# Kernel tuning notes

Hardware: AMD Instinct MI355X
Metric: run time of the kernel (lower is better)

## Reference

```python
import jax, jax.numpy as jnp
import numpy as np

B, N, E = 2, 16000, 160000
NDIMS, NMEAS, NMODES = 2, 1, 128
IN_DIM, OUT_DIM, FC_DIM = 3, 1, 128
LAYERS = [64, 64, 64, 64]
INV_MIN, INV_MAX = 0.5, 2.0


def setup_inputs() -> dict:
    key = jax.random.key(0)
    ks = jax.random.split(key, 16)
    L = len(LAYERS) - 1
    C = LAYERS[0]
    scale = 1.0 / (C * C)
    u = lambda k, sh, s: jax.random.uniform(k, sh, jnp.float32, -s, s)
    inp = {}
    inp["x"] = jax.random.normal(ks[0], (B, N, IN_DIM), jnp.float32)
    inp["node_mask"] = jnp.ones((B, N, 1), jnp.int32)
    inp["nodes"] = jax.random.uniform(ks[1], (B, N, NDIMS), jnp.float32)
    inp["node_weights"] = jax.random.uniform(ks[2], (B, N, NMEAS), jnp.float32) / N
    inp["directed_edges"] = jax.random.randint(ks[3], (B, E, 2), 0, N, jnp.int32)
    inp["edge_gradient_weights"] = jax.random.normal(ks[4], (B, E, NDIMS), jnp.float32)
    inp["modes"] = jax.random.normal(ks[5], (NMODES, NDIMS, NMEAS), jnp.float32)
    # scaled_logit(1.0, 0.5, 2.0) = log(0.5/1.0)
    inp["inv_L_scale_latent"] = jnp.full((NDIMS, NMEAS), np.log((1.0 - INV_MIN) / (INV_MAX - 1.0)), jnp.float32)
    inp["fc0_W"] = u(ks[6], (C, IN_DIM), 1.0 / np.sqrt(IN_DIM))
    inp["fc0_b"] = jnp.zeros((C,), jnp.float32)
    inp["weights_c"] = u(ks[7], (L, C, C, NMODES, NMEAS), scale)
    inp["weights_s"] = u(ks[8], (L, C, C, NMODES, NMEAS), scale)
    inp["weights_0"] = u(ks[9], (L, C, C, 1, NMEAS), scale)
    inp["ws_W"] = u(ks[10], (L, C, C), 1.0 / np.sqrt(C))
    inp["ws_b"] = jnp.zeros((L, C), jnp.float32)
    inp["gws_W"] = u(ks[11], (L, C, C * NDIMS), 1.0 / np.sqrt(C * NDIMS))
    inp["gws_b"] = jnp.zeros((L, C), jnp.float32)
    inp["fc1_W"] = u(ks[12], (FC_DIM, C), 1.0 / np.sqrt(C))
    inp["fc1_b"] = jnp.zeros((FC_DIM,), jnp.float32)
    inp["fc2_W"] = u(ks[13], (OUT_DIM, FC_DIM), 1.0 / np.sqrt(FC_DIM))
    inp["fc2_b"] = jnp.zeros((OUT_DIM,), jnp.float32)
    return inp


def _forward(x, nodes, node_weights, edge_gradient_weights, modes, inv_L_scale_latent,
             fc0_W, fc0_b, weights_c, weights_s, weights_0, ws_W, ws_b, gws_W, gws_b,
             fc1_W, fc1_b, fc2_W, fc2_b, directed_edges):
    L = weights_c.shape[0]
    n = x.shape[1]
    # scaled sigmoid of latent inverse length scale
    inv_L = INV_MIN + (INV_MAX - INV_MIN) * jax.nn.sigmoid(inv_L_scale_latent)
    smodes = modes * inv_L  # [K, D, W]
    # Fourier bases over all nodes
    temp = jnp.einsum('bxd,kdw->bxkw', nodes, smodes)  # [B, N, K, W]
    bases_c, bases_s = jnp.cos(temp), jnp.sin(temp)
    bases_0 = jnp.ones(temp.shape[:2] + (1, temp.shape[-1]), temp.dtype)
    wnw = node_weights[:, :, None, :]  # [B, N, 1, W]
    wbases_c, wbases_s, wbases_0 = bases_c * wnw, bases_s * wnw, bases_0 * wnw

    tgt = directed_edges[..., 0]  # [B, E]
    src = directed_edges[..., 1]

    def grad_field(f):  # f: [B, C, N] -> [B, C*D, N]
        ft = jnp.transpose(f, (0, 2, 1))  # [B, N, C]
        f_src = jnp.take_along_axis(ft, src[..., None], axis=1)  # [B, E, C]
        f_tgt = jnp.take_along_axis(ft, tgt[..., None], axis=1)
        diff = f_src - f_tgt
        msg = jnp.einsum('bed,bec->becd', edge_gradient_weights, diff)  # [B, E, C, D]
        msg = msg.reshape(msg.shape[0], msg.shape[1], -1)  # [B, E, C*D]
        seg = jax.vmap(lambda m, t: jax.ops.segment_sum(m, t, num_segments=n))(msg, tgt)
        return jnp.transpose(seg, (0, 2, 1))  # [B, C*D, N]

    # lift: fc0 acts on channel dim
    h = jnp.einsum('oi,bni->bon', fc0_W, x) + fc0_b[None, :, None]  # [B, C, N]

    for i in range(L):
        # spectral conv with explicit bases
        x_c = jnp.einsum('bix,bxkw->bikw', h, wbases_c)
        x_s = -jnp.einsum('bix,bxkw->bikw', h, wbases_s)
        x_0 = jnp.einsum('bix,bxkw->bikw', h, wbases_0)
        f_c = jnp.einsum('bikw,iokw->bokw', x_c, weights_c[i]) - jnp.einsum('bikw,iokw->bokw', x_s, weights_s[i])
        f_s = jnp.einsum('bikw,iokw->bokw', x_s, weights_c[i]) + jnp.einsum('bikw,iokw->bokw', x_c, weights_s[i])
        f_0 = jnp.einsum('bikw,iokw->bokw', x_0, weights_0[i])
        x1 = (jnp.einsum('bokw,bxkw->box', f_0, bases_0)
              + 2 * jnp.einsum('bokw,bxkw->box', f_c, bases_c)
              - 2 * jnp.einsum('bokw,bxkw->box', f_s, bases_s))
        # pointwise linear W
        x2 = jnp.einsum('oi,bin->bon', ws_W[i], h) + ws_b[i][None, :, None]
        # differential operator D: gradient then linear
        x3 = jnp.einsum('oi,bin->bon', gws_W[i], grad_field(h)) + gws_b[i][None, :, None]
        h = x1 + x2 + x3
        if i < L - 1:
            h = jax.nn.gelu(h)

    out = jnp.transpose(h, (0, 2, 1))  # [B, N, C]
    out = jax.nn.gelu(jnp.einsum('oc,bnc->bno', fc1_W, out) + fc1_b)
    out = jnp.einsum('oc,bnc->bno', fc2_W, out) + fc2_b
    return out  # [B, N, out_dim]


def reference(x, node_mask, nodes, node_weights, directed_edges, edge_gradient_weights,
              modes, inv_L_scale_latent, fc0_W, fc0_b, weights_c, weights_s, weights_0,
              ws_W, ws_b, gws_W, gws_b, fc1_W, fc1_b, fc2_W, fc2_b):
    del node_mask  # padding mask; all-ones here, not used in the core math
    return _forward(x, nodes, node_weights, edge_gradient_weights, modes, inv_L_scale_latent,
                    fc0_W, fc0_b, weights_c, weights_s, weights_0, ws_W, ws_b, gws_W, gws_b,
                    fc1_W, fc1_b, fc2_W, fc2_b, directed_edges)
```

## Files before the change

### kernel.cpp

```cpp
#include <hip/hip_runtime.h>
#include <math.h>

#define BB 2
#define NN 16000
#define EE 160000
#define KK 128
#define CC 64
#define LL 3

typedef __attribute__((ext_vector_type(8))) short bf16x8;
typedef __attribute__((ext_vector_type(4))) float f32x4;

__device__ __forceinline__ float gelu_f(float x){
    float x3 = x * x * x;
    return 0.5f * x * (1.f + tanhf(0.7978845608028654f * (x + 0.044715f * x3)));
}
__device__ __forceinline__ ushort f2bf(float f){
    uint u = __float_as_uint(f);
    u += 0x7fff + ((u >> 16) & 1);
    return (ushort)(u >> 16);
}
__device__ __forceinline__ float bf2f(ushort h){ return __uint_as_float(((uint)h) << 16); }
__device__ __forceinline__ void fsplit(float v, ushort &hi, ushort &lo){
    hi = f2bf(v);
    lo = f2bf(v - bf2f(hi));
}
__device__ __forceinline__ uint pk2(ushort a, ushort b){ return (uint)a | ((uint)b << 16); }

__global__ __launch_bounds__(256) void k_bases(
    const float* __restrict__ nodes, const float* __restrict__ modes,
    const float* __restrict__ latent, const float* __restrict__ nw,
    ushort* __restrict__ cbh, ushort* __restrict__ cbl,
    ushort* __restrict__ sbh, ushort* __restrict__ sbl,
    ushort* __restrict__ wTh, ushort* __restrict__ wTl){
    int bid = blockIdx.x;
    int b = bid / 250, x0 = (bid % 250) * 64;
    int t = threadIdx.x;
    __shared__ float sm0[128], sm1[128], nwv[64];
    __shared__ uint tc[64][65], ts[64][65];
    if (t < 128){
        float i0 = 0.5f + 1.5f / (1.f + expf(-latent[0]));
        float i1 = 0.5f + 1.5f / (1.f + expf(-latent[1]));
        sm0[t] = modes[t*2+0] * i0;
        sm1[t] = modes[t*2+1] * i1;
    }
    if (t < 64) nwv[t] = nw[b*NN + x0 + t];
    __syncthreads();
    int xloc = t & 63;
    float n0 = nodes[((size_t)b*NN + x0 + xloc)*2 + 0];
    float n1 = nodes[((size_t)b*NN + x0 + xloc)*2 + 1];
    for (int kh = 0; kh < 2; kh++){
        int kq = t >> 6;
        #pragma unroll
        for (int j = 0; j < 16; j++){
            int kl = kq*16 + j;
            int k = kh*64 + kl;
            float tmp = n0*sm0[k] + n1*sm1[k];
            float sv, cv; sincosf(tmp, &sv, &cv);
            ushort h_, l_;
            fsplit(cv, h_, l_); tc[xloc][kl] = pk2(h_, l_);
            fsplit(sv, h_, l_); ts[xloc][kl] = pk2(h_, l_);
        }
        __syncthreads();
        {
            int q = t >> 6;
            size_t base = ((size_t)b*NN + x0 + xloc)*128 + kh*64 + q*16;
            #pragma unroll
            for (int g2 = 0; g2 < 2; g2++){
                uint u0 = tc[xloc][q*16 + g2*8 + 0], u1 = tc[xloc][q*16 + g2*8 + 1];
                uint u2 = tc[xloc][q*16 + g2*8 + 2], u3 = tc[xloc][q*16 + g2*8 + 3];
                uint u4 = tc[xloc][q*16 + g2*8 + 4], u5 = tc[xloc][q*16 + g2*8 + 5];
                uint u6 = tc[xloc][q*16 + g2*8 + 6], u7 = tc[xloc][q*16 + g2*8 + 7];
                uint4 vh, vl;
                vh.x = pk2((ushort)u0,(ushort)u1); vh.y = pk2((ushort)u2,(ushort)u3);
                vh.z = pk2((ushort)u4,(ushort)u5); vh.w = pk2((ushort)u6,(ushort)u7);
                vl.x = pk2((ushort)(u0>>16),(ushort)(u1>>16)); vl.y = pk2((ushort)(u2>>16),(ushort)(u3>>16));
                vl.z = pk2((ushort)(u4>>16),(ushort)(u5>>16)); vl.w = pk2((ushort)(u6>>16),(ushort)(u7>>16));
                *(uint4*)&cbh[base + g2*8] = vh;
                *(uint4*)&cbl[base + g2*8] = vl;
                u0 = ts[xloc][q*16 + g2*8 + 0]; u1 = ts[xloc][q*16 + g2*8 + 1];
                u2 = ts[xloc][q*16 + g2*8 + 2]; u3 = ts[xloc][q*16 + g2*8 + 3];
                u4 = ts[xloc][q*16 + g2*8 + 4]; u5 = ts[xloc][q*16 + g2*8 + 5];
                u6 = ts[xloc][q*16 + g2*8 + 6]; u7 = ts[xloc][q*16 + g2*8 + 7];
                vh.x = pk2((ushort)u0,(ushort)u1); vh.y = pk2((ushort)u2,(ushort)u3);
                vh.z = pk2((ushort)u4,(ushort)u5); vh.w = pk2((ushort)u6,(ushort)u7);
                vl.x = pk2((ushort)(u0>>16),(ushort)(u1>>16)); vl.y = pk2((ushort)(u2>>16),(ushort)(u3>>16));
                vl.z = pk2((ushort)(u4>>16),(ushort)(u5>>16)); vl.w = pk2((ushort)(u6>>16),(ushort)(u7>>16));
                *(uint4*)&sbh[base + g2*8] = vh;
                *(uint4*)&sbl[base + g2*8] = vl;
            }
        }
        {
            int k = t & 63, g = t >> 6;
            int kgc = kh*64 + k;
            int kgs = 128 + kh*64 + k;
            ushort hc[16], lc[16], hs[16], ls[16];
            #pragma unroll
            for (int j = 0; j < 16; j++){
                int xx = g*16 + j;
                float wgt = nwv[xx];
                uint uc = tc[xx][k], us = ts[xx][k];
                float vc = (bf2f((ushort)uc) + bf2f((ushort)(uc>>16))) * wgt;
                float vs = (bf2f((ushort)us) + bf2f((ushort)(us>>16))) * wgt;
                fsplit(vc, hc[j], lc[j]);
                fsplit(vs, hs[j], ls[j]);
            }
            size_t wbc = ((size_t)b*256 + kgc)*16000 + x0 + g*16;
            size_t wbs = ((size_t)b*256 + kgs)*16000 + x0 + g*16;
            uint4 v;
            v.x = pk2(hc[0],hc[1]); v.y = pk2(hc[2],hc[3]); v.z = pk2(hc[4],hc[5]); v.w = pk2(hc[6],hc[7]);
            *(uint4*)&wTh[wbc] = v;
            v.x = pk2(hc[8],hc[9]); v.y = pk2(hc[10],hc[11]); v.z = pk2(hc[12],hc[13]); v.w = pk2(hc[14],hc[15]);
            *(uint4*)&wTh[wbc + 8] = v;
            v.x = pk2(lc[0],lc[1]); v.y = pk2(lc[2],lc[3]); v.z = pk2(lc[4],lc[5]); v.w = pk2(lc[6],lc[7]);
            *(uint4*)&wTl[wbc] = v;
            v.x = pk2(lc[8],lc[9]); v.y = pk2(lc[10],lc[11]); v.z = pk2(lc[12],lc[13]); v.w = pk2(lc[14],lc[15]);
            *(uint4*)&wTl[wbc + 8] = v;
            v.x = pk2(hs[0],hs[1]); v.y = pk2(hs[2],hs[3]); v.z = pk2(hs[4],hs[5]); v.w = pk2(hs[6],hs[7]);
            *(uint4*)&wTh[wbs] = v;
            v.x = pk2(hs[8],hs[9]); v.y = pk2(hs[10],hs[11]); v.z = pk2(hs[12],hs[13]); v.w = pk2(hs[14],hs[15]);
            *(uint4*)&wTh[wbs + 8] = v;
            v.x = pk2(ls[0],ls[1]); v.y = pk2(ls[2],ls[3]); v.z = pk2(ls[4],ls[5]); v.w = pk2(ls[6],ls[7]);
            *(uint4*)&wTl[wbs] = v;
            v.x = pk2(ls[8],ls[9]); v.y = pk2(ls[10],ls[11]); v.z = pk2(ls[12],ls[13]); v.w = pk2(ls[14],ls[15]);
            *(uint4*)&wTl[wbs + 8] = v;
        }
        __syncthreads();
    }
}

__device__ __forceinline__ void write_h_outputs(
    const float* ot, const float* nws, int b, int s, int x0, int t, int doAux,
    float* __restrict__ hx, ushort* __restrict__ hxh, ushort* __restrict__ hxl,
    ushort* __restrict__ hwh, ushort* __restrict__ hwl, float* __restrict__ part0){
    {
        int xl = t >> 1, half = t & 1;
        size_t gb = ((size_t)b*NN + x0 + xl)*64 + half*32;
        const float* row = &ot[xl*68 + half*32];
        #pragma unroll
        for (int j = 0; j < 8; j++){
            float4 v; v.x = row[j*4]; v.y = row[j*4+1]; v.z = row[j*4+2]; v.w = row[j*4+3];
            *(float4*)&hx[gb + j*4] = v;
        }
        if (doAux){
            #pragma unroll
            for (int q = 0; q < 4; q++){
                ushort h_[8], l_[8];
                #pragma unroll
                for (int j = 0; j < 8; j++) fsplit(row[q*8 + j], h_[j], l_[j]);
                uint4 vh, vl;
                vh.x = pk2(h_[0],h_[1]); vh.y = pk2(h_[2],h_[3]); vh.z = pk2(h_[4],h_[5]); vh.w = pk2(h_[6],h_[7]);
                vl.x = pk2(l_[0],l_[1]); vl.y = pk2(l_[2],l_[3]); vl.z = pk2(l_[4],l_[5]); vl.w = pk2(l_[6],l_[7]);
                *(uint4*)&hxh[gb + q*8] = vh;
                *(uint4*)&hxl[gb + q*8] = vl;
            }
        }
    }
    if (doAux){
        int i = t & 63, g = t >> 6;
        float a = 0.f;
        #pragma unroll
        for (int rep = 0; rep < 4; rep++){
            int xs = g*32 + rep*8;
            ushort h_[8], l_[8];
            #pragma unroll
            for (int j = 0; j < 8; j++){
                float v = ot[(xs + j)*68 + i] * nws[xs + j];
                a += v;
                fsplit(v, h_[j], l_[j]);
            }
            uint4 vh, vl;
            vh.x = pk2(h_[0],h_[1]); vh.y = pk2(h_[2],h_[3]); vh.z = pk2(h_[4],h_[5]); vh.w = pk2(h_[6],h_[7]);
            vl.x = pk2(l_[0],l_[1]); vl.y = pk2(l_[2],l_[3]); vl.z = pk2(l_[4],l_[5]); vl.w = pk2(l_[6],l_[7]);
            size_t wb = (size_t)(b*64 + i)*16000 + x0 + xs;
            *(uint4*)&hwh[wb] = vh;
            *(uint4*)&hwl[wb] = vl;
        }
        part0[((size_t)(b*125 + s)*4 + g)*64 + i] = a;
    }
}

__global__ __launch_bounds__(256) void k_fc0(
    const float* __restrict__ x, const float* __restrict__ W,
    const float* __restrict__ bb, const float* __restrict__ nw,
    float* __restrict__ hx, ushort* __restrict__ hxh, ushort* __restrict__ hxl,
    ushort* __restrict__ hwh, ushort* __restrict__ hwl, float* __restrict__ part0){
    int bid = blockIdx.x;
    int b = bid / 125, s = bid % 125;
    int x0 = s * 128;
    int t = threadIdx.x;
    __shared__ float ot[128*68];
    __shared__ float nws[128];
    __shared__ float Wf[192], bf_[64];
    if (t < 192) Wf[t] = W[t];
    if (t < 64) bf_[t] = bb[t];
    if (t < 128) nws[t] = nw[b*NN + x0 + t];
    __syncthreads();
    {
        int xl = t >> 1, half = t & 1;
        float v0 = x[((size_t)b*NN + x0 + xl)*3 + 0];
        float v1 = x[((size_t)b*NN + x0 + xl)*3 + 1];
        float v2 = x[((size_t)b*NN + x0 + xl)*3 + 2];
        #pragma unroll
        for (int j = 0; j < 32; j++){
            int o = half*32 + j;
            ot[xl*68 + o] = Wf[o*3]*v0 + Wf[o*3+1]*v1 + Wf[o*3+2]*v2 + bf_[o];
        }
    }
    __syncthreads();
    write_h_outputs(ot, nws, b, s, x0, t, 1, hx, hxh, hxl, hwh, hwl, part0);
}

__global__ __launch_bounds__(256) void csr_hist(
    const int* __restrict__ edges, int* __restrict__ cnt){
    int idx = blockIdx.x * 256 + threadIdx.x;
    if (idx >= BB*EE) return;
    int b = idx / EE;
    int tgt = edges[(size_t)idx*2];
    atomicAdd(&cnt[b*NN + tgt], 1);
}

__global__ __launch_bounds__(1024) void csr_scan(
    const int* __restrict__ cnt, int* __restrict__ rowptr, int* __restrict__ cursor){
    int b = blockIdx.x;
    int t = threadIdx.x;
    __shared__ int lds[1024];
    int base = t * 16;
    int v[16];
    int run = 0;
    #pragma unroll
    for (int j = 0; j < 16; j++){
        int n = base + j;
        int c = (n < NN) ? cnt[b*NN + n] : 0;
        v[j] = run;
        run += c;
    }
    lds[t] = run;
    __syncthreads();
    for (int off = 1; off < 1024; off <<= 1){
        int xv = (t >= off) ? lds[t-off] : 0;
        __syncthreads();
        lds[t] += xv;
        __syncthreads();
    }
    int toff = lds[t] - run;
    #pragma unroll
    for (int j = 0; j < 16; j++){
        int n = base + j;
        if (n < NN){
            int p = toff + v[j];
            rowptr[b*(NN+1) + n] = p;
            cursor[b*NN + n] = p;
        }
    }
    if (t == 1023) rowptr[b*(NN+1) + NN] = lds[1023];
}

__global__ __launch_bounds__(256) void csr_fill(
    const int* __restrict__ edges, const float* __restrict__ egw,
    int* __restrict__ cursor, int* __restrict__ insrc, float2* __restrict__ inw){
    int idx = blockIdx.x * 256 + threadIdx.x;
    if (idx >= BB*EE) return;
    int b = idx / EE;
    int tgt = edges[(size_t)idx*2];
    int src = edges[(size_t)idx*2 + 1];
    int pos = atomicAdd(&cursor[b*NN + tgt], 1);
    insrc[(size_t)b*EE + pos] = src;
    const float2 wv = *(const float2*)&egw[(size_t)idx*2];
    inw[(size_t)b*EE + pos] = wv;
}

__global__ __launch_bounds__(256) void k1_fwd(
    const ushort* __restrict__ hwH, const ushort* __restrict__ hwL,
    const ushort* __restrict__ wTH, const ushort* __restrict__ wTL,
    float* __restrict__ part){
    int bid = blockIdx.x;
    int b = bid / 250, s = bid % 250;
    int x0 = s * 64;
    int t = threadIdx.x, l = t & 63, w = t >> 6;
    __shared__ __align__(16) ushort Bh[128*64], Bl[128*64];
    f32x4 acc[16] = {};
    bf16x8 Ah[2], Al[2];
    int i = w*16 + (l & 15);
    #pragma unroll
    for (int ks = 0; ks < 2; ks++){
        size_t ab = (size_t)(b*64 + i)*16000 + x0 + ks*32 + ((l >> 4) * 8);
        Ah[ks] = *reinterpret_cast<const bf16x8*>(&hwH[ab]);
        Al[ks] = *reinterpret_cast<const bf16x8*>(&hwL[ab]);
    }
    for (int p = 0; p < 2; p++){
        #pragma unroll
        for (int it = 0; it < 4; it++){
            int u = it*256 + t;
            int kloc = u >> 3, q = u & 7;
            size_t g = ((size_t)(b*256 + p*128 + kloc))*16000 + x0 + q*8;
            uint4 vh = *(const uint4*)&wTH[g];
            uint4 vl = *(const uint4*)&wTL[g];
            int ldsb = kloc*128 + ((q*16) ^ ((kloc & 7) << 4));
            *(uint4*)&Bh[ldsb >> 1] = vh;
            *(uint4*)&Bl[ldsb >> 1] = vl;
        }
        __syncthreads();
        #pragma unroll
        for (int kt = 0; kt < 8; kt++){
            int kcol = kt*16 + (l & 15);
            int ai = p*8 + kt;
            #pragma unroll
            for (int ks = 0; ks < 2; ks++){
                int boff = kcol*128 + (((ks*64) + ((l >> 4) * 16)) ^ ((kcol & 7) << 4));
                bf16x8 bh = *reinterpret_cast<const bf16x8*>(&Bh[boff >> 1]);
                bf16x8 bl = *reinterpret_cast<const bf16x8*>(&Bl[boff >> 1]);
                acc[ai] = __builtin_amdgcn_mfma_f32_16x16x32_bf16(Ah[ks], bh, acc[ai], 0, 0, 0);
                acc[ai] = __builtin_amdgcn_mfma_f32_16x16x32_bf16(Ah[ks], bl, acc[ai], 0, 0, 0);
                acc[ai] = __builtin_amdgcn_mfma_f32_16x16x32_bf16(Al[ks], bh, acc[ai], 0, 0, 0);
            }
        }
        __syncthreads();
    }
    size_t pb = (size_t)(b*250 + s) * 64 * 256;
    #pragma unroll
    for (int nt = 0; nt < 16; nt++){
        #pragma unroll
        for (int r = 0; r < 4; r++){
            int irow = w*16 + (l >> 4)*4 + r;
            part[pb + (size_t)irow*256 + nt*16 + (l & 15)] = acc[nt][r];
        }
    }
}

__global__ __launch_bounds__(512) void k1_reduce(
    const float* __restrict__ part, float* __restrict__ Sc, float* __restrict__ Ss){
    int b = blockIdx.x >> 6, i = blockIdx.x & 63;
    int t = threadIdx.x;
    int c = t & 255, sh = t >> 8;
    float a0=0,a1=0,a2=0,a3=0;
    int j = sh;
    for (; j + 6 < 250; j += 8){
        a0 += part[((size_t)(b*250 + j    )*64 + i)*256 + c];
        a1 += part[((size_t)(b*250 + j + 2)*64 + i)*256 + c];
        a2 += part[((size_t)(b*250 + j + 4)*64 + i)*256 + c];
        a3 += part[((size_t)(b*250 + j + 6)*64 + i)*256 + c];
    }
    for (; j < 250; j += 2)
        a0 += part[((size_t)(b*250 + j)*64 + i)*256 + c];
    float sum = (a0+a1)+(a2+a3);
    __shared__ float r2[256];
    if (sh) r2[c] = sum;
    __syncthreads();
    if (!sh){
        sum += r2[c];
        if (c < 128) Sc[(size_t)(b*64 + i)*128 + c] = sum;
        else         Ss[(size_t)(b*64 + i)*128 + (c - 128)] = sum;
    }
}

__global__ __launch_bounds__(256) void k2_mix(
    const float* __restrict__ Sc, const float* __restrict__ Ss,
    const float* __restrict__ part0,
    const float* __restrict__ wc, const float* __restrict__ wsp,
    const float* __restrict__ w0,
    const float* __restrict__ wsb, const float* __restrict__ gwsb,
    const float* __restrict__ wsW, const float* __restrict__ gwsW,
    ushort* __restrict__ WbH, ushort* __restrict__ WbL,
    float* __restrict__ bias, int l){
    int b = blockIdx.x >> 6, o = blockIdx.x & 63;
    int t = threadIdx.x;
    __shared__ float fc2s[2][128], fs2s[2][128];
    __shared__ float red[64];
    if (t < 64){
        float x0 = 0.f;
        for (int s2 = 0; s2 < 500; s2++) x0 += part0[(size_t)(b*500 + s2)*64 + t];
        red[t] = x0 * w0[((size_t)l*CC + t)*CC + o];
    }
    int k = t & 127, hf = t >> 7;
    float fc = 0.f, fs = 0.f;
    for (int i = hf*32; i < hf*32 + 32; i++){
        float sc = Sc[(size_t)(b*CC + i)*KK + k];
        float ss = Ss[(size_t)(b*CC + i)*KK + k];
        size_t wi = (((size_t)l*CC + i)*CC + o)*KK + k;
        float a = wc[wi], bb2 = wsp[wi];
        fc += sc*a + ss*bb2;
        fs += sc*bb2 - ss*a;
    }
    fc2s[hf][k] = fc; fs2s[hf][k] = fs;
    __syncthreads();
    size_t wb = (size_t)(b*CC + o) * 448;
    if (t < 128){
        float FC = fc2s[0][t] + fc2s[1][t];
        float FS = fs2s[0][t] + fs2s[1][t];
        ushort h_, l_;
        fsplit(2.f*FC, h_, l_);
        WbH[wb + t] = h_; WbL[wb + t] = l_;
        fsplit(-2.f*FS, h_, l_);
        WbH[wb + 128 + t] = h_; WbL[wb + 128 + t] = l_;
    }
    if (t < 192){
        float v = (t < 64) ? wsW[((size_t)l*CC + o)*CC + t]
                           : gwsW[((size_t)l*CC + o)*128 + (t - 64)];
        ushort h_, l_; fsplit(v, h_, l_);
        WbH[wb + 256 + t] = h_; WbL[wb + 256 + t] = l_;
    }
    if (t == 0){
        float f0 = 0.f;
        for (int i = 0; i < 64; i++) f0 += red[i];
        bias[b*CC + o] = f0 + wsb[l*CC + o] + gwsb[l*CC + o];
    }
}

__global__ __launch_bounds__(256) void k_grad(
    const float* __restrict__ h, const int* __restrict__ rowptr,
    const int* __restrict__ insrc, const float2* __restrict__ inw,
    ushort* __restrict__ segh, ushort* __restrict__ segl){
    int bid = blockIdx.x;
    int b = bid / 2000, n0 = (bid % 2000) * 8;
    int w = threadIdx.x >> 6, c = threadIdx.x & 63;
    const float*  hb  = h + (size_t)b*NN*CC;
    const int*    isb = insrc + (size_t)b*EE;
    const float2* iwb = inw + (size_t)b*EE;
    #pragma unroll
    for (int g = 0; g < 2; g++){
        int n = n0 + w*2 + g;
        float hn = hb[(size_t)n*CC + c];
        int p0 = rowptr[b*(NN+1) + n];
        int p1 = rowptr[b*(NN+1) + n + 1];
        float a0 = 0.f, a1 = 0.f;
        int p = p0;
        for (; p + 4 <= p1; p += 4){
            int s0 = isb[p], s1 = isb[p+1], s2 = isb[p+2], s3 = isb[p+3];
            float2 w0 = iwb[p], w1 = iwb[p+1], w2 = iwb[p+2], w3 = iwb[p+3];
            float d0 = hb[(size_t)s0*CC + c] - hn;
            float d1 = hb[(size_t)s1*CC + c] - hn;
            float d2 = hb[(size_t)s2*CC + c] - hn;
            float d3 = hb[(size_t)s3*CC + c] - hn;
            a0 += w0.x*d0 + w1.x*d1 + w2.x*d2 + w3.x*d3;
            a1 += w0.y*d0 + w1.y*d1 + w2.y*d2 + w3.y*d3;
        }
        for (; p < p1; p++){
            int sx = isb[p]; float2 ww = iwb[p];
            float d = hb[(size_t)sx*CC + c] - hn;
            a0 += ww.x*d; a1 += ww.y*d;
        }
        ushort h0_, l0_, h1_, l1_;
        fsplit(a0, h0_, l0_);
        fsplit(a1, h1_, l1_);
        size_t sb2 = ((size_t)b*NN + n)*128 + 2*c;
        *(uint*)&segh[sb2] = pk2(h0_, h1_);
        *(uint*)&segl[sb2] = pk2(l0_, l1_);
    }
}

__global__ __launch_bounds__(256) void k3_gemm(
    const ushort* __restrict__ WbH, const ushort* __restrict__ WbL,
    const float* __restrict__ bias,
    const ushort* __restrict__ cbh, const ushort* __restrict__ cbl,
    const ushort* __restrict__ sbh, const ushort* __restrict__ sbl,
    const ushort* __restrict__ hxh, const ushort* __restrict__ hxl,
    const ushort* __restrict__ sgh, const ushort* __restrict__ sgl,
    const float* __restrict__ nw,
    float* __restrict__ hxO, ushort* __restrict__ hxhO, ushort* __restrict__ hxlO,
    ushort* __restrict__ hwhO, ushort* __restrict__ hwlO, float* __restrict__ part0,
    int doAux){
    int bid = blockIdx.x;
    int b = bid / 125, s = bid % 125, x0 = s * 128;
    int t = threadIdx.x, l = t & 63, w = t >> 6;
    __shared__ __align__(16) char smem[34816];
    ushort* Vh = (ushort*)smem;
    ushort* Vl = Vh + 8192;
    __shared__ float nws[128];
    if (t < 128) nws[t] = nw[b*NN + x0 + t];
    f32x4 acc[8] = {};
    int o = w*16 + (l & 15);
    for (int cc = 0; cc < 7; cc++){
        const ushort *srcH, *srcL; int rl, co;
        switch (cc){
            case 0:  srcH = cbh; srcL = cbl; rl = 128; co = 0;  break;
            case 1:  srcH = cbh; srcL = cbl; rl = 128; co = 64; break;
            case 2:  srcH = sbh; srcL = sbl; rl = 128; co = 0;  break;
            case 3:  srcH = sbh; srcL = sbl; rl = 128; co = 64; break;
            case 4:  srcH = hxh; srcL = hxl; rl = 64;  co = 0;  break;
            case 5:  srcH = sgh; srcL = sgl; rl = 128; co = 0;  break;
            default: srcH = sgh; srcL = sgl; rl = 128; co = 64; break;
        }
        __syncthreads();
        #pragma unroll
        for (int it = 0; it < 4; it++){
            int u = it*256 + t;
            int xl2 = u >> 3, q = u & 7;
            size_t g = (size_t)(b*NN + x0 + xl2)*rl + co + q*8;
            uint4 vh = *(const uint4*)&srcH[g];
            uint4 vl2 = *(const uint4*)&srcL[g];
            int ldsb = xl2*128 + ((q*16) ^ ((xl2 & 7) << 4));
            *(uint4*)&Vh[ldsb >> 1] = vh;
            *(uint4*)&Vl[ldsb >> 1] = vl2;
        }
        __syncthreads();
        bf16x8 Ah[2], Al[2];
        #pragma unroll
        for (int ks = 0; ks < 2; ks++){
            size_t ab = (size_t)(b*64 + o)*448 + cc*64 + ks*32 + ((l >> 4) * 8);
            Ah[ks] = *reinterpret_cast<const bf16x8*>(&WbH[ab]);
            Al[ks] = *reinterpret_cast<const bf16x8*>(&WbL[ab]);
        }
        #pragma unroll
        for (int nt = 0; nt < 8; nt++){
            int xc = nt*16 + (l & 15);
            #pragma unroll
            for (int ks = 0; ks < 2; ks++){
                int boff = xc*128 + (((ks*64) + ((l >> 4) * 16)) ^ ((xc & 7) << 4));
                bf16x8 bh = *reinterpret_cast<const bf16x8*>(&Vh[boff >> 1]);
                bf16x8 bl = *reinterpret_cast<const bf16x8*>(&Vl[boff >> 1]);
                acc[nt] = __builtin_amdgcn_mfma_f32_16x16x32_bf16(Ah[ks], bh, acc[nt], 0, 0, 0);
                acc[nt] = __builtin_amdgcn_mfma_f32_16x16x32_bf16(Ah[ks], bl, acc[nt], 0, 0, 0);
                acc[nt] = __builtin_amdgcn_mfma_f32_16x16x32_bf16(Al[ks], bh, acc[nt], 0, 0, 0);
            }
        }
    }
    __syncthreads();
    float* ot = (float*)smem;
    float bv[4];
    #pragma unroll
    for (int r = 0; r < 4; r++) bv[r] = bias[b*64 + w*16 + (l >> 4)*4 + r];
    #pragma unroll
    for (int nt = 0; nt < 8; nt++){
        int xc = nt*16 + (l & 15);
        #pragma unroll
        for (int r = 0; r < 4; r++){
            float v = acc[nt][r] + bv[r];
            if (doAux) v = gelu_f(v);
            ot[xc*68 + (w*16 + (l >> 4)*4 + r)] = v;
        }
    }
    __syncthreads();
    write_h_outputs(ot, nws, b, s, x0, t, doAux, hxO, hxhO, hxlO, hwhO, hwlO, part0);
}

__global__ __launch_bounds__(256) void k_head(
    const float* __restrict__ h, const float* __restrict__ W1,
    const float* __restrict__ b1, const float* __restrict__ W2,
    const float* __restrict__ b2, float* __restrict__ out){
    int bid = blockIdx.x;
    int b = bid / 250, n0 = (bid % 250) * 64;
    int t = threadIdx.x, w = t >> 6, f = t & 63;
    __shared__ float Wl[128][65];
    #pragma unroll
    for (int r = 0; r < 8; r++){
        int u = r*256 + t;
        int ff = u >> 4, cq = u & 15;
        float4 v = *(const float4*)&W1[ff*64 + cq*4];
        Wl[ff][cq*4+0] = v.x; Wl[ff][cq*4+1] = v.y;
        Wl[ff][cq*4+2] = v.z; Wl[ff][cq*4+3] = v.w;
    }
    __syncthreads();
    float w2a = W2[f], w2b = W2[64+f];
    float b1a = b1[f], b1b = b1[64+f];
    float b2v = b2[0];
    for (int g = 0; g < 16; g++){
        int n = n0 + w*16 + g;
        float hv = h[((size_t)b*NN + n)*CC + f];
        float a1 = b1a, a2 = b1b;
        #pragma unroll
        for (int c2 = 0; c2 < 64; c2++){
            float xv = __shfl(hv, c2, 64);
            a1 += Wl[f][c2] * xv;
            a2 += Wl[64+f][c2] * xv;
        }
        float p = gelu_f(a1)*w2a + gelu_f(a2)*w2b;
        for (int off = 32; off; off >>= 1) p += __shfl_down(p, off, 64);
        if (f == 0) out[(size_t)b*NN + n] = p + b2v;
    }
}

extern "C" void kernel_launch(void* const* d_in, const int* in_sizes, int n_in,
                              void* d_out, int out_size, void* d_ws, size_t ws_size,
                              hipStream_t stream){
    const float* x_in  = (const float*)d_in[0];
    const float* nodes = (const float*)d_in[2];
    const float* nw    = (const float*)d_in[3];
    const int*   edges = (const int*)d_in[4];
    const float* egw   = (const float*)d_in[5];
    const float* modes = (const float*)d_in[6];
    const float* latent= (const float*)d_in[7];
    const float* fc0W  = (const float*)d_in[8];
    const float* fc0b  = (const float*)d_in[9];
    const float* wc    = (const float*)d_in[10];
    const float* wsp   = (const float*)d_in[11];
    const float* w0    = (const float*)d_in[12];
    const float* wsW   = (const float*)d_in[13];
    const float* wsb   = (const float*)d_in[14];
    const float* gwsW  = (const float*)d_in[15];
    const float* gwsb  = (const float*)d_in[16];
    const float* fc1W  = (const float*)d_in[17];
    const float* fc1b  = (const float*)d_in[18];
    const float* fc2W  = (const float*)d_in[19];
    const float* fc2b  = (const float*)d_in[20];
    float* out = (float*)d_out;

    char* wsbase = (char*)d_ws;
    size_t off = 0;
    auto alloc = [&](size_t bytes) -> void* {
        void* p = wsbase + off;
        off += (bytes + 255) & ~(size_t)255;
        return p;
    };
    ushort* cbh = (ushort*)alloc((size_t)BB*NN*128*2);
    ushort* cbl = (ushort*)alloc((size_t)BB*NN*128*2);
    ushort* sbh = (ushort*)alloc((size_t)BB*NN*128*2);
    ushort* sbl = (ushort*)alloc((size_t)BB*NN*128*2);
    ushort* wTh = (ushort*)alloc((size_t)BB*256*NN*2);
    ushort* wTl = (ushort*)alloc((size_t)BB*256*NN*2);
    float*  hx[2];  ushort* hxh[2]; ushort* hxl[2]; ushort* hwh[2]; ushort* hwl[2];
    for (int i = 0; i < 2; i++){
        hx[i]  = (float*) alloc((size_t)BB*NN*64*4);
        hxh[i] = (ushort*)alloc((size_t)BB*NN*64*2);
        hxl[i] = (ushort*)alloc((size_t)BB*NN*64*2);
        hwh[i] = (ushort*)alloc((size_t)BB*64*NN*2);
        hwl[i] = (ushort*)alloc((size_t)BB*64*NN*2);
    }
    ushort* segh = (ushort*)alloc((size_t)BB*NN*128*2);
    ushort* segl = (ushort*)alloc((size_t)BB*NN*128*2);
    float*  part = (float*) alloc((size_t)BB*250*64*256*4);
    float*  part0= (float*) alloc((size_t)BB*125*4*64*4);
    float*  Sc   = (float*) alloc((size_t)BB*64*128*4);
    float*  Ss   = (float*) alloc((size_t)BB*64*128*4);
    ushort* WbH  = (ushort*)alloc((size_t)BB*64*448*2);
    ushort* WbL  = (ushort*)alloc((size_t)BB*64*448*2);
    float*  bias = (float*) alloc((size_t)BB*64*4);
    int*   cnt   = (int*)   alloc((size_t)BB*NN*4);
    int*   rowptr= (int*)   alloc((size_t)BB*(NN+4)*4);
    int*   cursor= (int*)   alloc((size_t)BB*NN*4);
    int*   insrc = (int*)   alloc((size_t)BB*EE*4);
    float2* inw  = (float2*)alloc((size_t)BB*EE*8);

    k_bases<<<BB*250, 256, 0, stream>>>(nodes, modes, latent, nw,
                                        cbh, cbl, sbh, sbl, wTh, wTl);
    k_fc0<<<BB*125, 256, 0, stream>>>(x_in, fc0W, fc0b, nw,
                                      hx[0], hxh[0], hxl[0], hwh[0], hwl[0], part0);

    hipMemsetAsync(cnt, 0, (size_t)BB*NN*4, stream);
    csr_hist<<<(BB*EE+255)/256, 256, 0, stream>>>(edges, cnt);
    csr_scan<<<BB, 1024, 0, stream>>>(cnt, rowptr, cursor);
    csr_fill<<<(BB*EE+255)/256, 256, 0, stream>>>(edges, egw, cursor, insrc, inw);

    int cur = 0;
    for (int l = 0; l < LL; l++){
        int nxt = cur ^ 1;
        int doAux = (l < LL-1) ? 1 : 0;
        k1_fwd<<<BB*250, 256, 0, stream>>>(hwh[cur], hwl[cur], wTh, wTl, part);
        k1_reduce<<<BB*64, 512, 0, stream>>>(part, Sc, Ss);
        k2_mix<<<BB*64, 256, 0, stream>>>(Sc, Ss, part0, wc, wsp, w0, wsb, gwsb,
                                          wsW, gwsW, WbH, WbL, bias, l);
        k_grad<<<BB*2000, 256, 0, stream>>>(hx[cur], rowptr, insrc, inw, segh, segl);
        k3_gemm<<<BB*125, 256, 0, stream>>>(WbH, WbL, bias,
                                            cbh, cbl, sbh, sbl,
                                            hxh[cur], hxl[cur], segh, segl, nw,
                                            hx[nxt], hxh[nxt], hxl[nxt],
                                            hwh[nxt], hwl[nxt], part0, doAux);
        cur = nxt;
    }
    k_head<<<BB*250, 256, 0, stream>>>(hx[cur], fc1W, fc1b, fc2W, fc2b, out);
    (void)in_sizes; (void)n_in; (void)out_size; (void)ws_size; (void)segh; (void)segl;
}
```

Measured before the change: 509.2 us.

## Merge independent kernels into multi-role launches and parallelize mix reductions

Combines the basis-generation, fc0 and counter-zeroing work into one launch with block-index role dispatch, and fuses the spectral forward GEMM with the gradient gather kernel per layer so both run concurrently in a single grid. k2_mix's part0 reduction is spread over 256 threads instead of 64, and the weight-packing writes are split across more threads. The aim is fewer launches and better overlap of independent work. In exchange, the merged kernels share the larger LDS allocation across all roles, which may lower occupancy for the lighter roles.

```diff
diff --git a/kernel.cpp b/kernel.cpp
--- a/kernel.cpp
+++ b/kernel.cpp
@@ -27,17 +27,71 @@
 }
 __device__ __forceinline__ uint pk2(ushort a, ushort b){ return (uint)a | ((uint)b << 16); }
 
-__global__ __launch_bounds__(256) void k_bases(
+__device__ __forceinline__ void write_h_outputs(
+    const float* ot, const float* nws, int b, int s, int x0, int t, int doAux,
+    float* __restrict__ hx, ushort* __restrict__ hxh, ushort* __restrict__ hxl,
+    ushort* __restrict__ hwh, ushort* __restrict__ hwl, float* __restrict__ part0){
+    {
+        int xl = t >> 1, half = t & 1;
+        size_t gb = ((size_t)b*NN + x0 + xl)*64 + half*32;
+        const float* row = &ot[xl*68 + half*32];
+        #pragma unroll
+        for (int j = 0; j < 8; j++){
+            float4 v; v.x = row[j*4]; v.y = row[j*4+1]; v.z = row[j*4+2]; v.w = row[j*4+3];
+            *(float4*)&hx[gb + j*4] = v;
+        }
+        if (doAux){
+            #pragma unroll
+            for (int q = 0; q < 4; q++){
+                ushort h_[8], l_[8];
+                #pragma unroll
+                for (int j = 0; j < 8; j++) fsplit(row[q*8 + j], h_[j], l_[j]);
+                uint4 vh, vl;
+                vh.x = pk2(h_[0],h_[1]); vh.y = pk2(h_[2],h_[3]); vh.z = pk2(h_[4],h_[5]); vh.w = pk2(h_[6],h_[7]);
+                vl.x = pk2(l_[0],l_[1]); vl.y = pk2(l_[2],l_[3]); vl.z = pk2(l_[4],l_[5]); vl.w = pk2(l_[6],l_[7]);
+                *(uint4*)&hxh[gb + q*8] = vh;
+                *(uint4*)&hxl[gb + q*8] = vl;
+            }
+        }
+    }
+    if (doAux){
+        int i = t & 63, g = t >> 6;
+        float a = 0.f;
+        #pragma unroll
+        for (int rep = 0; rep < 4; rep++){
+            int xs = g*32 + rep*8;
+            ushort h_[8], l_[8];
+            #pragma unroll
+            for (int j = 0; j < 8; j++){
+                float v = ot[(xs + j)*68 + i] * nws[xs + j];
+                a += v;
+                fsplit(v, h_[j], l_[j]);
+            }
+            uint4 vh, vl;
+            vh.x = pk2(h_[0],h_[1]); vh.y = pk2(h_[2],h_[3]); vh.z = pk2(h_[4],h_[5]); vh.w = pk2(h_[6],h_[7]);
+            vl.x = pk2(l_[0],l_[1]); vl.y = pk2(l_[2],l_[3]); vl.z = pk2(l_[4],l_[5]); vl.w = pk2(l_[6],l_[7]);
+            size_t wb = (size_t)(b*64 + i)*16000 + x0 + xs;
+            *(uint4*)&hwh[wb] = vh;
+            *(uint4*)&hwl[wb] = vl;
+        }
+        part0[((size_t)(b*125 + s)*4 + g)*64 + i] = a;
+    }
+}
+
+__device__ void bases_role(
+    int bid, char* smem,
     const float* __restrict__ nodes, const float* __restrict__ modes,
     const float* __restrict__ latent, const float* __restrict__ nw,
     ushort* __restrict__ cbh, ushort* __restrict__ cbl,
     ushort* __restrict__ sbh, ushort* __restrict__ sbl,
     ushort* __restrict__ wTh, ushort* __restrict__ wTl){
-    int bid = blockIdx.x;
     int b = bid / 250, x0 = (bid % 250) * 64;
     int t = threadIdx.x;
-    __shared__ float sm0[128], sm1[128], nwv[64];
-    __shared__ uint tc[64][65], ts[64][65];
+    float* sm0 = (float*)smem;
+    float* sm1 = sm0 + 128;
+    float* nwv = sm1 + 128;
+    uint* tc = (uint*)(nwv + 64);
+    uint* ts = tc + 64*65;
     if (t < 128){
         float i0 = 0.5f + 1.5f / (1.f + expf(-latent[0]));
         float i1 = 0.5f + 1.5f / (1.f + expf(-latent[1]));
@@ -58,8 +112,8 @@
             float tmp = n0*sm0[k] + n1*sm1[k];
             float sv, cv; sincosf(tmp, &sv, &cv);
             ushort h_, l_;
-            fsplit(cv, h_, l_); tc[xloc][kl] = pk2(h_, l_);
-            fsplit(sv, h_, l_); ts[xloc][kl] = pk2(h_, l_);
+            fsplit(cv, h_, l_); tc[xloc*65 + kl] = pk2(h_, l_);
+            fsplit(sv, h_, l_); ts[xloc*65 + kl] = pk2(h_, l_);
         }
         __syncthreads();
         {
@@ -67,10 +121,10 @@
             size_t base = ((size_t)b*NN + x0 + xloc)*128 + kh*64 + q*16;
             #pragma unroll
             for (int g2 = 0; g2 < 2; g2++){
-                uint u0 = tc[xloc][q*16 + g2*8 + 0], u1 = tc[xloc][q*16 + g2*8 + 1];
-                uint u2 = tc[xloc][q*16 + g2*8 + 2], u3 = tc[xloc][q*16 + g2*8 + 3];
-                uint u4 = tc[xloc][q*16 + g2*8 + 4], u5 = tc[xloc][q*16 + g2*8 + 5];
-                uint u6 = tc[xloc][q*16 + g2*8 + 6], u7 = tc[xloc][q*16 + g2*8 + 7];
+                uint u0 = tc[xloc*65 + q*16 + g2*8 + 0], u1 = tc[xloc*65 + q*16 + g2*8 + 1];
+                uint u2 = tc[xloc*65 + q*16 + g2*8 + 2], u3 = tc[xloc*65 + q*16 + g2*8 + 3];
+                uint u4 = tc[xloc*65 + q*16 + g2*8 + 4], u5 = tc[xloc*65 + q*16 + g2*8 + 5];
+                uint u6 = tc[xloc*65 + q*16 + g2*8 + 6], u7 = tc[xloc*65 + q*16 + g2*8 + 7];
                 uint4 vh, vl;
                 vh.x = pk2((ushort)u0,(ushort)u1); vh.y = pk2((ushort)u2,(ushort)u3);
                 vh.z = pk2((ushort)u4,(ushort)u5); vh.w = pk2((ushort)u6,(ushort)u7);
@@ -78,10 +132,10 @@
                 vl.z = pk2((ushort)(u4>>16),(ushort)(u5>>16)); vl.w = pk2((ushort)(u6>>16),(ushort)(u7>>16));
                 *(uint4*)&cbh[base + g2*8] = vh;
                 *(uint4*)&cbl[base + g2*8] = vl;
-                u0 = ts[xloc][q*16 + g2*8 + 0]; u1 = ts[xloc][q*16 + g2*8 + 1];
-                u2 = ts[xloc][q*16 + g2*8 + 2]; u3 = ts[xloc][q*16 + g2*8 + 3];
-                u4 = ts[xloc][q*16 + g2*8 + 4]; u5 = ts[xloc][q*16 + g2*8 + 5];
-                u6 = ts[xloc][q*16 + g2*8 + 6]; u7 = ts[xloc][q*16 + g2*8 + 7];
+                u0 = ts[xloc*65 + q*16 + g2*8 + 0]; u1 = ts[xloc*65 + q*16 + g2*8 + 1];
+                u2 = ts[xloc*65 + q*16 + g2*8 + 2]; u3 = ts[xloc*65 + q*16 + g2*8 + 3];
+                u4 = ts[xloc*65 + q*16 + g2*8 + 4]; u5 = ts[xloc*65 + q*16 + g2*8 + 5];
+                u6 = ts[xloc*65 + q*16 + g2*8 + 6]; u7 = ts[xloc*65 + q*16 + g2*8 + 7];
                 vh.x = pk2((ushort)u0,(ushort)u1); vh.y = pk2((ushort)u2,(ushort)u3);
                 vh.z = pk2((ushort)u4,(ushort)u5); vh.w = pk2((ushort)u6,(ushort)u7);
                 vl.x = pk2((ushort)(u0>>16),(ushort)(u1>>16)); vl.y = pk2((ushort)(u2>>16),(ushort)(u3>>16));
@@ -99,7 +153,7 @@
             for (int j = 0; j < 16; j++){
                 int xx = g*16 + j;
                 float wgt = nwv[xx];
-                uint uc = tc[xx][k], us = ts[xx][k];
+                uint uc = tc[xx*65 + k], us = ts[xx*65 + k];
                 float vc = (bf2f((ushort)uc) + bf2f((ushort)(uc>>16))) * wgt;
                 float vs = (bf2f((ushort)us) + bf2f((ushort)(us>>16))) * wgt;
                 fsplit(vc, hc[j], lc[j]);
@@ -129,69 +183,19 @@
     }
 }
 
-__device__ __forceinline__ void write_h_outputs(
-    const float* ot, const float* nws, int b, int s, int x0, int t, int doAux,
-    float* __restrict__ hx, ushort* __restrict__ hxh, ushort* __restrict__ hxl,
-    ushort* __restrict__ hwh, ushort* __restrict__ hwl, float* __restrict__ part0){
-    {
-        int xl = t >> 1, half = t & 1;
-        size_t gb = ((size_t)b*NN + x0 + xl)*64 + half*32;
-        const float* row = &ot[xl*68 + half*32];
-        #pragma unroll
-        for (int j = 0; j < 8; j++){
-            float4 v; v.x = row[j*4]; v.y = row[j*4+1]; v.z = row[j*4+2]; v.w = row[j*4+3];
-            *(float4*)&hx[gb + j*4] = v;
-        }
-        if (doAux){
-            #pragma unroll
-            for (int q = 0; q < 4; q++){
-                ushort h_[8], l_[8];
-                #pragma unroll
-                for (int j = 0; j < 8; j++) fsplit(row[q*8 + j], h_[j], l_[j]);
-                uint4 vh, vl;
-                vh.x = pk2(h_[0],h_[1]); vh.y = pk2(h_[2],h_[3]); vh.z = pk2(h_[4],h_[5]); vh.w = pk2(h_[6],h_[7]);
-                vl.x = pk2(l_[0],l_[1]); vl.y = pk2(l_[2],l_[3]); vl.z = pk2(l_[4],l_[5]); vl.w = pk2(l_[6],l_[7]);
-                *(uint4*)&hxh[gb + q*8] = vh;
-                *(uint4*)&hxl[gb + q*8] = vl;
-            }
-        }
-    }
-    if (doAux){
-        int i = t & 63, g = t >> 6;
-        float a = 0.f;
-        #pragma unroll
-        for (int rep = 0; rep < 4; rep++){
-            int xs = g*32 + rep*8;
-            ushort h_[8], l_[8];
-            #pragma unroll
-            for (int j = 0; j < 8; j++){
-                float v = ot[(xs + j)*68 + i] * nws[xs + j];
-                a += v;
-                fsplit(v, h_[j], l_[j]);
-            }
-            uint4 vh, vl;
-            vh.x = pk2(h_[0],h_[1]); vh.y = pk2(h_[2],h_[3]); vh.z = pk2(h_[4],h_[5]); vh.w = pk2(h_[6],h_[7]);
-            vl.x = pk2(l_[0],l_[1]); vl.y = pk2(l_[2],l_[3]); vl.z = pk2(l_[4],l_[5]); vl.w = pk2(l_[6],l_[7]);
-            size_t wb = (size_t)(b*64 + i)*16000 + x0 + xs;
-            *(uint4*)&hwh[wb] = vh;
-            *(uint4*)&hwl[wb] = vl;
-        }
-        part0[((size_t)(b*125 + s)*4 + g)*64 + i] = a;
-    }
-}
-
-__global__ __launch_bounds__(256) void k_fc0(
+__device__ void fc0_role(
+    int bid, char* smem,
     const float* __restrict__ x, const float* __restrict__ W,
     const float* __restrict__ bb, const float* __restrict__ nw,
     float* __restrict__ hx, ushort* __restrict__ hxh, ushort* __restrict__ hxl,
     ushort* __restrict__ hwh, ushort* __restrict__ hwl, float* __restrict__ part0){
-    int bid = blockIdx.x;
     int b = bid / 125, s = bid % 125;
     int x0 = s * 128;
     int t = threadIdx.x;
-    __shared__ float ot[128*68];
-    __shared__ float nws[128];
-    __shared__ float Wf[192], bf_[64];
+    float* ot  = (float*)smem;
+    float* nws = ot + 128*68;
+    float* Wf  = nws + 128;
+    float* bf_ = Wf + 192;
     if (t < 192) Wf[t] = W[t];
     if (t < 64) bf_[t] = bb[t];
     if (t < 128) nws[t] = nw[b*NN + x0 + t];
@@ -209,6 +213,29 @@
     }
     __syncthreads();
     write_h_outputs(ot, nws, b, s, x0, t, 1, hx, hxh, hxl, hwh, hwl, part0);
+}
+
+__global__ __launch_bounds__(256) void k_start(
+    const float* __restrict__ nodes, const float* __restrict__ modes,
+    const float* __restrict__ latent, const float* __restrict__ nw,
+    const float* __restrict__ x, const float* __restrict__ fc0W,
+    const float* __restrict__ fc0b,
+    ushort* __restrict__ cbh, ushort* __restrict__ cbl,
+    ushort* __restrict__ sbh, ushort* __restrict__ sbl,
+    ushort* __restrict__ wTh, ushort* __restrict__ wTl,
+    float* __restrict__ hx, ushort* __restrict__ hxh, ushort* __restrict__ hxl,
+    ushort* __restrict__ hwh, ushort* __restrict__ hwl, float* __restrict__ part0,
+    int* __restrict__ cnt){
+    __shared__ __align__(16) char smem[36864];
+    int bid = blockIdx.x;
+    if (bid < BB*250){
+        bases_role(bid, smem, nodes, modes, latent, nw, cbh, cbl, sbh, sbl, wTh, wTl);
+    } else if (bid < BB*250 + BB*125){
+        fc0_role(bid - BB*250, smem, x, fc0W, fc0b, nw, hx, hxh, hxl, hwh, hwl, part0);
+    } else {
+        int idx = (bid - (BB*250 + BB*125))*256 + threadIdx.x;
+        cnt[idx] = 0;
+    }
 }
 
 __global__ __launch_bounds__(256) void csr_hist(
@@ -270,15 +297,16 @@
     inw[(size_t)b*EE + pos] = wv;
 }
 
-__global__ __launch_bounds__(256) void k1_fwd(
+__device__ void fwd_role(
+    int bid, char* smem,
     const ushort* __restrict__ hwH, const ushort* __restrict__ hwL,
     const ushort* __restrict__ wTH, const ushort* __restrict__ wTL,
     float* __restrict__ part){
-    int bid = blockIdx.x;
     int b = bid / 250, s = bid % 250;
     int x0 = s * 64;
     int t = threadIdx.x, l = t & 63, w = t >> 6;
-    __shared__ __align__(16) ushort Bh[128*64], Bl[128*64];
+    ushort* Bh = (ushort*)smem;
+    ushort* Bl = Bh + 128*64;
     f32x4 acc[16] = {};
     bf16x8 Ah[2], Al[2];
     int i = w*16 + (l & 15);
@@ -289,6 +317,7 @@
         Al[ks] = *reinterpret_cast<const bf16x8*>(&hwL[ab]);
     }
     for (int p = 0; p < 2; p++){
+        if (p) __syncthreads();
         #pragma unroll
         for (int it = 0; it < 4; it++){
             int u = it*256 + t;
@@ -315,7 +344,6 @@
                 acc[ai] = __builtin_amdgcn_mfma_f32_16x16x32_bf16(Al[ks], bh, acc[ai], 0, 0, 0);
             }
         }
-        __syncthreads();
     }
     size_t pb = (size_t)(b*250 + s) * 64 * 256;
     #pragma unroll
@@ -328,90 +356,11 @@
     }
 }
 
-__global__ __launch_bounds__(512) void k1_reduce(
-    const float* __restrict__ part, float* __restrict__ Sc, float* __restrict__ Ss){
-    int b = blockIdx.x >> 6, i = blockIdx.x & 63;
-    int t = threadIdx.x;
-    int c = t & 255, sh = t >> 8;
-    float a0=0,a1=0,a2=0,a3=0;
-    int j = sh;
-    for (; j + 6 < 250; j += 8){
-        a0 += part[((size_t)(b*250 + j    )*64 + i)*256 + c];
-        a1 += part[((size_t)(b*250 + j + 2)*64 + i)*256 + c];
-        a2 += part[((size_t)(b*250 + j + 4)*64 + i)*256 + c];
-        a3 += part[((size_t)(b*250 + j + 6)*64 + i)*256 + c];
-    }
-    for (; j < 250; j += 2)
-        a0 += part[((size_t)(b*250 + j)*64 + i)*256 + c];
-    float sum = (a0+a1)+(a2+a3);
-    __shared__ float r2[256];
-    if (sh) r2[c] = sum;
-    __syncthreads();
-    if (!sh){
-        sum += r2[c];
-        if (c < 128) Sc[(size_t)(b*64 + i)*128 + c] = sum;
-        else         Ss[(size_t)(b*64 + i)*128 + (c - 128)] = sum;
-    }
-}
-
-__global__ __launch_bounds__(256) void k2_mix(
-    const float* __restrict__ Sc, const float* __restrict__ Ss,
-    const float* __restrict__ part0,
-    const float* __restrict__ wc, const float* __restrict__ wsp,
-    const float* __restrict__ w0,
-    const float* __restrict__ wsb, const float* __restrict__ gwsb,
-    const float* __restrict__ wsW, const float* __restrict__ gwsW,
-    ushort* __restrict__ WbH, ushort* __restrict__ WbL,
-    float* __restrict__ bias, int l){
-    int b = blockIdx.x >> 6, o = blockIdx.x & 63;
-    int t = threadIdx.x;
-    __shared__ float fc2s[2][128], fs2s[2][128];
-    __shared__ float red[64];
-    if (t < 64){
-        float x0 = 0.f;
-        for (int s2 = 0; s2 < 500; s2++) x0 += part0[(size_t)(b*500 + s2)*64 + t];
-        red[t] = x0 * w0[((size_t)l*CC + t)*CC + o];
-    }
-    int k = t & 127, hf = t >> 7;
-    float fc = 0.f, fs = 0.f;
-    for (int i = hf*32; i < hf*32 + 32; i++){
-        float sc = Sc[(size_t)(b*CC + i)*KK + k];
-        float ss = Ss[(size_t)(b*CC + i)*KK + k];
-        size_t wi = (((size_t)l*CC + i)*CC + o)*KK + k;
-        float a = wc[wi], bb2 = wsp[wi];
-        fc += sc*a + ss*bb2;
-        fs += sc*bb2 - ss*a;
-    }
-    fc2s[hf][k] = fc; fs2s[hf][k] = fs;
-    __syncthreads();
-    size_t wb = (size_t)(b*CC + o) * 448;
-    if (t < 128){
-        float FC = fc2s[0][t] + fc2s[1][t];
-        float FS = fs2s[0][t] + fs2s[1][t];
-        ushort h_, l_;
-        fsplit(2.f*FC, h_, l_);
-        WbH[wb + t] = h_; WbL[wb + t] = l_;
-        fsplit(-2.f*FS, h_, l_);
-        WbH[wb + 128 + t] = h_; WbL[wb + 128 + t] = l_;
-    }
-    if (t < 192){
-        float v = (t < 64) ? wsW[((size_t)l*CC + o)*CC + t]
-                           : gwsW[((size_t)l*CC + o)*128 + (t - 64)];
-        ushort h_, l_; fsplit(v, h_, l_);
-        WbH[wb + 256 + t] = h_; WbL[wb + 256 + t] = l_;
-    }
-    if (t == 0){
-        float f0 = 0.f;
-        for (int i = 0; i < 64; i++) f0 += red[i];
-        bias[b*CC + o] = f0 + wsb[l*CC + o] + gwsb[l*CC + o];
-    }
-}
-
-__global__ __launch_bounds__(256) void k_grad(
+__device__ void grad_role(
+    int bid,
     const float* __restrict__ h, const int* __restrict__ rowptr,
     const int* __restrict__ insrc, const float2* __restrict__ inw,
     ushort* __restrict__ segh, ushort* __restrict__ segl){
-    int bid = blockIdx.x;
     int b = bid / 2000, n0 = (bid % 2000) * 8;
     int w = threadIdx.x >> 6, c = threadIdx.x & 63;
     const float*  hb  = h + (size_t)b*NN*CC;
@@ -446,6 +395,113 @@
         size_t sb2 = ((size_t)b*NN + n)*128 + 2*c;
         *(uint*)&segh[sb2] = pk2(h0_, h1_);
         *(uint*)&segl[sb2] = pk2(l0_, l1_);
+    }
+}
+
+__global__ __launch_bounds__(256) void k_layer1(
+    const ushort* __restrict__ hwH, const ushort* __restrict__ hwL,
+    const ushort* __restrict__ wTH, const ushort* __restrict__ wTL,
+    float* __restrict__ part,
+    const float* __restrict__ hxcur, const int* __restrict__ rowptr,
+    const int* __restrict__ insrc, const float2* __restrict__ inw,
+    ushort* __restrict__ segh, ushort* __restrict__ segl){
+    __shared__ __align__(16) char smem[32768];
+    int bid = blockIdx.x;
+    if (bid < BB*250){
+        fwd_role(bid, smem, hwH, hwL, wTH, wTL, part);
+    } else {
+        grad_role(bid - BB*250, hxcur, rowptr, insrc, inw, segh, segl);
+    }
+}
+
+__global__ __launch_bounds__(512) void k1_reduce(
+    const float* __restrict__ part, float* __restrict__ Sc, float* __restrict__ Ss){
+    int b = blockIdx.x >> 6, i = blockIdx.x & 63;
+    int t = threadIdx.x;
+    int c = t & 255, sh = t >> 8;
+    float a0=0,a1=0,a2=0,a3=0;
+    int j = sh;
+    for (; j + 6 < 250; j += 8){
+        a0 += part[((size_t)(b*250 + j    )*64 + i)*256 + c];
+        a1 += part[((size_t)(b*250 + j + 2)*64 + i)*256 + c];
+        a2 += part[((size_t)(b*250 + j + 4)*64 + i)*256 + c];
+        a3 += part[((size_t)(b*250 + j + 6)*64 + i)*256 + c];
+    }
+    for (; j < 250; j += 2)
+        a0 += part[((size_t)(b*250 + j)*64 + i)*256 + c];
+    float sum = (a0+a1)+(a2+a3);
+    __shared__ float r2[256];
+    if (sh) r2[c] = sum;
+    __syncthreads();
+    if (!sh){
+        sum += r2[c];
+        if (c < 128) Sc[(size_t)(b*64 + i)*128 + c] = sum;
+        else         Ss[(size_t)(b*64 + i)*128 + (c - 128)] = sum;
+    }
+}
+
+__global__ __launch_bounds__(256) void k2_mix(
+    const float* __restrict__ Sc, const float* __restrict__ Ss,
+    const float* __restrict__ part0,
+    const float* __restrict__ wc, const float* __restrict__ wsp,
+    const float* __restrict__ w0,
+    const float* __restrict__ wsb, const float* __restrict__ gwsb,
+    const float* __restrict__ wsW, const float* __restrict__ gwsW,
+    ushort* __restrict__ WbH, ushort* __restrict__ WbL,
+    float* __restrict__ bias, int l){
+    int b = blockIdx.x >> 6, o = blockIdx.x & 63;
+    int t = threadIdx.x;
+    __shared__ float fc2s[2][128], fs2s[2][128];
+    __shared__ float redp[4][64];
+    __shared__ float red[64];
+    {
+        int i = t & 63, grp = t >> 6;
+        float a = 0.f;
+        for (int s2 = grp; s2 < 500; s2 += 4)
+            a += part0[(size_t)(b*500 + s2)*64 + i];
+        redp[grp][i] = a;
+    }
+    int k = t & 127, hf = t >> 7;
+    float fc = 0.f, fs = 0.f;
+    for (int i = hf*32; i < hf*32 + 32; i++){
+        float sc = Sc[(size_t)(b*CC + i)*KK + k];
+        float ss = Ss[(size_t)(b*CC + i)*KK + k];
+        size_t wi = (((size_t)l*CC + i)*CC + o)*KK + k;
+        float a = wc[wi], bb2 = wsp[wi];
+        fc += sc*a + ss*bb2;
+        fs += sc*bb2 - ss*a;
+    }
+    fc2s[hf][k] = fc; fs2s[hf][k] = fs;
+    __syncthreads();
+    if (t < 64)
+        red[t] = (redp[0][t]+redp[1][t]+redp[2][t]+redp[3][t]) * w0[((size_t)l*CC + t)*CC + o];
+    size_t wb = (size_t)(b*CC + o) * 448;
+    if (t < 128){
+        float FC = fc2s[0][t] + fc2s[1][t];
+        float FS = fs2s[0][t] + fs2s[1][t];
+        ushort h_, l_;
+        fsplit(2.f*FC, h_, l_);
+        WbH[wb + t] = h_; WbL[wb + t] = l_;
+        fsplit(-2.f*FS, h_, l_);
+        WbH[wb + 128 + t] = h_; WbL[wb + 128 + t] = l_;
+    }
+    if (t >= 128 && t < 192){
+        int q = t - 128;
+        float v = wsW[((size_t)l*CC + o)*CC + q];
+        ushort h_, l_; fsplit(v, h_, l_);
+        WbH[wb + 256 + q] = h_; WbL[wb + 256 + q] = l_;
+    }
+    if (t >= 128){
+        int q = t - 128;
+        float v = gwsW[((size_t)l*CC + o)*128 + q];
+        ushort h_, l_; fsplit(v, h_, l_);
+        WbH[wb + 320 + q] = h_; WbL[wb + 320 + q] = l_;
+    }
+    __syncthreads();
+    if (t == 0){
+        float f0 = 0.f;
+        for (int i = 0; i < 64; i++) f0 += red[i];
+        bias[b*CC + o] = f0 + wsb[l*CC + o] + gwsb[l*CC + o];
     }
 }
 
@@ -631,12 +687,11 @@
     int*   insrc = (int*)   alloc((size_t)BB*EE*4);
     float2* inw  = (float2*)alloc((size_t)BB*EE*8);
 
-    k_bases<<<BB*250, 256, 0, stream>>>(nodes, modes, latent, nw,
-                                        cbh, cbl, sbh, sbl, wTh, wTl);
-    k_fc0<<<BB*125, 256, 0, stream>>>(x_in, fc0W, fc0b, nw,
-                                      hx[0], hxh[0], hxl[0], hwh[0], hwl[0], part0);
-
-    hipMemsetAsync(cnt, 0, (size_t)BB*NN*4, stream);
+    k_start<<<BB*250 + BB*125 + 125, 256, 0, stream>>>(
+        nodes, modes, latent, nw, x_in, fc0W, fc0b,
+        cbh, cbl, sbh, sbl, wTh, wTl,
+        hx[0], hxh[0], hxl[0], hwh[0], hwl[0], part0, cnt);
+
     csr_hist<<<(BB*EE+255)/256, 256, 0, stream>>>(edges, cnt);
     csr_scan<<<BB, 1024, 0, stream>>>(cnt, rowptr, cursor);
     csr_fill<<<(BB*EE+255)/256, 256, 0, stream>>>(edges, egw, cursor, insrc, inw);
@@ -645,11 +700,12 @@
     for (int l = 0; l < LL; l++){
         int nxt = cur ^ 1;
         int doAux = (l < LL-1) ? 1 : 0;
-        k1_fwd<<<BB*250, 256, 0, stream>>>(hwh[cur], hwl[cur], wTh, wTl, part);
+        k_layer1<<<BB*250 + BB*2000, 256, 0, stream>>>(
+            hwh[cur], hwl[cur], wTh, wTl, part,
+            hx[cur], rowptr, insrc, inw, segh, segl);
         k1_reduce<<<BB*64, 512, 0, stream>>>(part, Sc, Ss);
         k2_mix<<<BB*64, 256, 0, stream>>>(Sc, Ss, part0, wc, wsp, w0, wsb, gwsb,
                                           wsW, gwsW, WbH, WbL, bias, l);
-        k_grad<<<BB*2000, 256, 0, stream>>>(hx[cur], rowptr, insrc, inw, segh, segl);
         k3_gemm<<<BB*125, 256, 0, stream>>>(WbH, WbL, bias,
                                             cbh, cbl, sbh, sbl,
                                             hxh[cur], hxl[cur], segh, segl, nw,
@@ -658,5 +714,5 @@
         cur = nxt;
     }
     k_head<<<BB*250, 256, 0, stream>>>(hx[cur], fc1W, fc1b, fc2W, fc2b, out);
-    (void)in_sizes; (void)n_in; (void)out_size; (void)ws_size; (void)segh; (void)segl;
-}
+    (void)in_sizes; (void)n_in; (void)out_size; (void)ws_size;
+}
```

Measured after the change: 578.7 us. 1.14x slower.
